# Kernel optimization log

Hardware: AMD Instinct MI355X
Metric: run time of the kernel (lower is better)

## Reference

```python
import jax, jax.numpy as jnp
import numpy as np

N = 100000   # nodes
E = 1600000  # edges (avg degree 16)
IN_DIM = 5
HID = 128
OUT_DIM = 1


def gcn_conv(x, src, dst, W, b, n):
    """PyG GCNConv: out = D^{-1/2}(A+I)D^{-1/2} (x @ W) + b, self-loops added."""
    h = x @ W  # [N, F_out]
    # degree including self-loop (edge weight 1 each)
    deg = jax.ops.segment_sum(jnp.ones(src.shape[0], h.dtype), dst, num_segments=n) + 1.0
    dinv = jax.lax.rsqrt(deg)  # deg >= 1 always (self-loop)
    coef = dinv[src] * dinv[dst]  # [E]
    agg = jax.ops.segment_sum(h[src] * coef[:, None], dst, num_segments=n)
    agg = agg + h * (dinv * dinv)[:, None]  # self-loop contribution
    return agg + b


def setup_inputs() -> dict:
    key = jax.random.key(0)
    k = jax.random.split(key, 6)
    x = jax.random.normal(k[0], (N, IN_DIM), jnp.float32)
    edge_index = jax.random.randint(k[1], (2, E), 0, N)
    W1 = jax.random.normal(k[2], (IN_DIM, HID), jnp.float32) / np.float32(np.sqrt(IN_DIM))
    b1 = jnp.zeros((HID,), jnp.float32)
    W2 = jax.random.normal(k[3], (HID, OUT_DIM), jnp.float32) / np.float32(np.sqrt(HID))
    b2 = jnp.zeros((OUT_DIM,), jnp.float32)
    return {"x": x, "edge_index": edge_index, "W1": W1, "b1": b1, "W2": W2, "b2": b2}


def reference(x, edge_index, W1, b1, W2, b2):
    src, dst = edge_index[0], edge_index[1]
    h = gcn_conv(x, src, dst, W1, b1, N)
    h = jax.nn.relu(h)
    out = gcn_conv(h, src, dst, W2, b2, N)
    return out
```

## Files before the change

### kernel.cpp

```cpp
#include <hip/hip_runtime.h>
#include <hip/hip_fp16.h>

#define Nn 100000
#define Ee 1600000
#define HID 128
#define IN_DIM 5

#define SH 8
#define BSZ 256
#define NB 391
#define BCAP 4608

#define PCHUNK 3125
#define PBLK 512
#define MAXK 7

typedef float f32x4 __attribute__((ext_vector_type(4)));
union F2H { float f; __half2 h; };

__global__ void zero_kernel(int* __restrict__ bcnt) {
    if (threadIdx.x < NB) bcnt[threadIdx.x] = 0;
}

__global__ __launch_bounds__(512) void partition_kernel(const int* __restrict__ src,
                                                        const int* __restrict__ dst,
                                                        unsigned int* __restrict__ recs,
                                                        int* __restrict__ bcnt) {
    __shared__ unsigned int stage[PCHUNK];
    __shared__ unsigned short bstage[PCHUNK];
    __shared__ int hist[NB + 1];
    __shared__ int histS[NB + 1];
    __shared__ int cur[NB];
    __shared__ int gbase[NB];
    __shared__ int wsum[8];
    int tid = threadIdx.x;
    int e0 = blockIdx.x * PCHUNK;
    for (int i = tid; i <= NB; i += 512) hist[i] = 0;
    __syncthreads();
    int rb[MAXK];
    unsigned int rv[MAXK];
    #pragma unroll
    for (int k = 0; k < MAXK; ++k) {
        int idx = tid + k * 512;
        rb[k] = -1;
        if (idx < PCHUNK) {
            int e = e0 + idx;
            int d = dst[e], s = src[e];
            rb[k] = d >> SH;
            rv[k] = ((unsigned int)(d & (BSZ - 1)) << 17) | (unsigned int)s;
            atomicAdd(&hist[rb[k]], 1);
        }
    }
    __syncthreads();
    int v = (tid < NB) ? hist[tid] : 0;
    int lane = tid & 63, wid = tid >> 6;
    int sc = v;
    #pragma unroll
    for (int ofs = 1; ofs < 64; ofs <<= 1) {
        int t = __shfl_up(sc, ofs, 64);
        if (lane >= ofs) sc += t;
    }
    if (lane == 63) wsum[wid] = sc;
    __syncthreads();
    int wpre = 0;
    #pragma unroll
    for (int w = 0; w < 8; ++w)
        if (w < wid) wpre += wsum[w];
    int excl = wpre + sc - v;
    if (tid < NB) {
        histS[tid] = excl;
        cur[tid] = excl;
        gbase[tid] = atomicAdd(&bcnt[tid], v);
    }
    __syncthreads();
    #pragma unroll
    for (int k = 0; k < MAXK; ++k)
        if (rb[k] >= 0) {
            int slot = atomicAdd(&cur[rb[k]], 1);
            stage[slot] = rv[k];
            bstage[slot] = (unsigned short)rb[k];
        }
    __syncthreads();
    for (int i = tid; i < PCHUNK; i += 512) {
        int b = bstage[i];
        recs[(size_t)b * BCAP + gbase[b] + (i - histS[b])] = stage[i];
    }
}

__global__ __launch_bounds__(BSZ) void sortk_kernel(const unsigned int* __restrict__ recs,
                                                    const int* __restrict__ bcnt,
                                                    const float* __restrict__ x,
                                                    int* __restrict__ degc,
                                                    unsigned int* __restrict__ nodeoff,
                                                    unsigned int* __restrict__ ssrc,
                                                    float* __restrict__ dinv,
                                                    f32x4* __restrict__ xd16) {
    __shared__ int cnt[BSZ];
    __shared__ int cur[BSZ];
    __shared__ int wsum[BSZ / 64];
    int b = blockIdx.x, tid = threadIdx.x;
    int n = bcnt[b];
    cnt[tid] = 0;
    __syncthreads();
    const unsigned int* R = recs + (size_t)b * BCAP;
    for (int i = tid; i < n; i += BSZ)
        atomicAdd(&cnt[R[i] >> 17], 1);
    __syncthreads();
    int v = cnt[tid];
    int lane = tid & 63, wid = tid >> 6;
    int sc = v;
    #pragma unroll
    for (int ofs = 1; ofs < 64; ofs <<= 1) {
        int t = __shfl_up(sc, ofs, 64);
        if (lane >= ofs) sc += t;
    }
    if (lane == 63) wsum[wid] = sc;
    __syncthreads();
    int wpre = 0;
    #pragma unroll
    for (int w = 0; w < BSZ / 64; ++w)
        if (w < wid) wpre += wsum[w];
    int excl = wpre + sc - v;
    cur[tid] = excl;
    int g = (b << SH) + tid;
    if (g < Nn) {
        degc[g] = v;
        nodeoff[g] = (unsigned int)(b * BCAP + excl);
        float di = rsqrtf((float)v + 1.0f);
        dinv[g] = di;
        f32x4 o;
        o.x = x[g * IN_DIM + 0] * di;
        o.y = x[g * IN_DIM + 1] * di;
        o.z = x[g * IN_DIM + 2] * di;
        F2H u;
        u.h = __floats2half2_rn(x[g * IN_DIM + 3] * di, x[g * IN_DIM + 4] * di);
        o.w = u.f;
        xd16[g] = o;
    }
    __syncthreads();
    unsigned int* O = ssrc + (size_t)b * BCAP;
    for (int i = tid; i < n; i += BSZ) {
        unsigned int r = R[i];
        int pos = atomicAdd(&cur[r >> 17], 1);
        O[pos] = r & 0x1FFFFu;
    }
}

__global__ __launch_bounds__(256) void gcn1_kernel(const unsigned int* __restrict__ ssrc,
                                                   const unsigned int* __restrict__ nodeoff,
                                                   const int* __restrict__ degc,
                                                   const f32x4* __restrict__ xd16,
                                                   const float* __restrict__ dinv,
                                                   const float* __restrict__ W1,
                                                   const float* __restrict__ b1,
                                                   const float* __restrict__ W2,
                                                   float* __restrict__ h2d) {
    __shared__ float w1s[IN_DIM * HID];
    __shared__ float w2s[HID], b1s[HID];
    int tid = threadIdx.x;
    for (int j = tid; j < IN_DIM * HID; j += 256) w1s[j] = W1[j];
    if (tid < HID) { w2s[tid] = W2[tid]; b1s[tid] = b1[tid]; }
    __syncthreads();
    int nd = blockIdx.x * 256 + tid;
    if (nd >= Nn) return;
    unsigned int off = nodeoff[nd];
    int len = degc[nd];
    float a0 = 0.f, a1 = 0.f, a2 = 0.f, a3 = 0.f, a4 = 0.f;
    int i = 0;
    for (; i + 4 <= len; i += 4) {
        unsigned int s0 = ssrc[off + i], s1 = ssrc[off + i + 1];
        unsigned int s2 = ssrc[off + i + 2], s3 = ssrc[off + i + 3];
        f32x4 v0 = xd16[s0], v1 = xd16[s1], v2 = xd16[s2], v3 = xd16[s3];
        F2H u0, u1, u2, u3;
        u0.f = v0.w; u1.f = v1.w; u2.f = v2.w; u3.f = v3.w;
        float2 e0 = __half22float2(u0.h), e1 = __half22float2(u1.h);
        float2 e2 = __half22float2(u2.h), e3 = __half22float2(u3.h);
        a0 += (v0.x + v1.x) + (v2.x + v3.x);
        a1 += (v0.y + v1.y) + (v2.y + v3.y);
        a2 += (v0.z + v1.z) + (v2.z + v3.z);
        a3 += (e0.x + e1.x) + (e2.x + e3.x);
        a4 += (e0.y + e1.y) + (e2.y + e3.y);
    }
    for (; i < len; ++i) {
        unsigned int s = ssrc[off + i];
        f32x4 v = xd16[s];
        F2H u; u.f = v.w; float2 e = __half22float2(u.h);
        a0 += v.x; a1 += v.y; a2 += v.z; a3 += e.x; a4 += e.y;
    }
    float di = dinv[nd];
    f32x4 sv = xd16[nd];
    F2H su; su.f = sv.w; float2 se = __half22float2(su.h);
    a0 = (a0 + sv.x) * di;
    a1 = (a1 + sv.y) * di;
    a2 = (a2 + sv.z) * di;
    a3 = (a3 + se.x) * di;
    a4 = (a4 + se.y) * di;
    float accp = 0.f;
    #pragma unroll
    for (int f = 0; f < HID; ++f) {
        float v = b1s[f] + a0 * w1s[f] + a1 * w1s[HID + f] + a2 * w1s[2 * HID + f]
                + a3 * w1s[3 * HID + f] + a4 * w1s[4 * HID + f];
        accp += fmaxf(v, 0.f) * w2s[f];
    }
    h2d[nd] = accp * di;
}

__global__ __launch_bounds__(256) void gcn2_kernel(const unsigned int* __restrict__ ssrc,
                                                   const unsigned int* __restrict__ nodeoff,
                                                   const int* __restrict__ degc,
                                                   const float* __restrict__ h2d,
                                                   const float* __restrict__ dinv,
                                                   const float* __restrict__ b2,
                                                   float* __restrict__ out) {
    int nd = blockIdx.x * 256 + threadIdx.x;
    if (nd >= Nn) return;
    unsigned int off = nodeoff[nd];
    int len = degc[nd];
    float s = 0.f;
    int i = 0;
    for (; i + 8 <= len; i += 8) {
        float t0 = h2d[ssrc[off + i]],     t1 = h2d[ssrc[off + i + 1]];
        float t2 = h2d[ssrc[off + i + 2]], t3 = h2d[ssrc[off + i + 3]];
        float t4 = h2d[ssrc[off + i + 4]], t5 = h2d[ssrc[off + i + 5]];
        float t6 = h2d[ssrc[off + i + 6]], t7 = h2d[ssrc[off + i + 7]];
        s += ((t0 + t1) + (t2 + t3)) + ((t4 + t5) + (t6 + t7));
    }
    for (; i < len; ++i) s += h2d[ssrc[off + i]];
    out[nd] = (s + h2d[nd]) * dinv[nd] + b2[0];
}

extern "C" void kernel_launch(void* const* d_in, const int* in_sizes, int n_in,
                              void* d_out, int out_size, void* d_ws, size_t ws_size,
                              hipStream_t stream) {
    const float* x  = (const float*)d_in[0];
    const int*   ei = (const int*)d_in[1];
    const float* W1 = (const float*)d_in[2];
    const float* b1 = (const float*)d_in[3];
    const float* W2 = (const float*)d_in[4];
    const float* b2 = (const float*)d_in[5];
    const int* src = ei;
    const int* dst = ei + Ee;
    float* out = (float*)d_out;

    float* dinv = (float*)d_ws;
    f32x4* xd16 = (f32x4*)(dinv + Nn);
    float* h2d  = (float*)(xd16 + Nn);
    int* degc   = (int*)(h2d + Nn);
    unsigned int* nodeoff = (unsigned int*)(degc + Nn);
    unsigned int* recs = nodeoff + Nn;
    unsigned int* ssrc = recs + (size_t)NB * BCAP;
    int* bcnt = (int*)(ssrc + (size_t)NB * BCAP);

    zero_kernel<<<1, 512, 0, stream>>>(bcnt);
    partition_kernel<<<PBLK, 512, 0, stream>>>(src, dst, recs, bcnt);
    sortk_kernel<<<NB, BSZ, 0, stream>>>(recs, bcnt, x, degc, nodeoff, ssrc, dinv, xd16);
    gcn1_kernel<<<(Nn + 255) / 256, 256, 0, stream>>>(ssrc, nodeoff, degc, xd16, dinv,
                                                      W1, b1, W2, h2d);
    gcn2_kernel<<<(Nn + 255) / 256, 256, 0, stream>>>(ssrc, nodeoff, degc, h2d, dinv, b2, out);
}
```

Measured before the change: 70.21 us.

## Build compact CSR via global degree atomics, block scan, and LDS-staged scatter

Per-node in-degrees are now counted with global atomics during partitioning instead of a per-bucket histogram pass. A new scan kernel assigns each 256-node block a base offset through an atomic allocator, giving a dense edge array with no per-bucket padding, and also computes dinv and the scaled features. The scatter kernel sorts bucket records into an LDS buffer and then writes them to global memory contiguously. The aim is to remove one read pass over the records, get coalesced writes and a compact CSR for the aggregation kernels. In exchange it adds 1.6M random global atomics and one more kernel launch.

```diff
diff --git a/kernel.cpp b/kernel.cpp
--- a/kernel.cpp
+++ b/kernel.cpp
@@ -18,12 +18,18 @@
 typedef float f32x4 __attribute__((ext_vector_type(4)));
 union F2H { float f; __half2 h; };
 
-__global__ void zero_kernel(int* __restrict__ bcnt) {
-    if (threadIdx.x < NB) bcnt[threadIdx.x] = 0;
+__global__ __launch_bounds__(256) void zero_kernel(int* __restrict__ degc,
+                                                   int* __restrict__ bcnt,
+                                                   unsigned int* __restrict__ galloc) {
+    int i = blockIdx.x * 256 + threadIdx.x;
+    if (i < Nn) degc[i] = 0;
+    if (i < NB) bcnt[i] = 0;
+    if (i == 0) *galloc = 0u;
 }
 
 __global__ __launch_bounds__(512) void partition_kernel(const int* __restrict__ src,
                                                         const int* __restrict__ dst,
+                                                        int* __restrict__ degc,
                                                         unsigned int* __restrict__ recs,
                                                         int* __restrict__ bcnt) {
     __shared__ unsigned int stage[PCHUNK];
@@ -46,6 +52,7 @@
         if (idx < PCHUNK) {
             int e = e0 + idx;
             int d = dst[e], s = src[e];
+            atomicAdd(&degc[d], 1);
             rb[k] = d >> SH;
             rv[k] = ((unsigned int)(d & (BSZ - 1)) << 17) | (unsigned int)s;
             atomicAdd(&hist[rb[k]], 1);
@@ -87,26 +94,17 @@
     }
 }
 
-__global__ __launch_bounds__(BSZ) void sortk_kernel(const unsigned int* __restrict__ recs,
-                                                    const int* __restrict__ bcnt,
-                                                    const float* __restrict__ x,
-                                                    int* __restrict__ degc,
-                                                    unsigned int* __restrict__ nodeoff,
-                                                    unsigned int* __restrict__ ssrc,
-                                                    float* __restrict__ dinv,
-                                                    f32x4* __restrict__ xd16) {
-    __shared__ int cnt[BSZ];
-    __shared__ int cur[BSZ];
-    __shared__ int wsum[BSZ / 64];
-    int b = blockIdx.x, tid = threadIdx.x;
-    int n = bcnt[b];
-    cnt[tid] = 0;
-    __syncthreads();
-    const unsigned int* R = recs + (size_t)b * BCAP;
-    for (int i = tid; i < n; i += BSZ)
-        atomicAdd(&cnt[R[i] >> 17], 1);
-    __syncthreads();
-    int v = cnt[tid];
+__global__ __launch_bounds__(256) void scan_prep_kernel(const int* __restrict__ degc,
+                                                        const float* __restrict__ x,
+                                                        unsigned int* __restrict__ nodeoff,
+                                                        float* __restrict__ dinv,
+                                                        f32x4* __restrict__ xd16,
+                                                        unsigned int* __restrict__ galloc) {
+    __shared__ int wsum[4];
+    __shared__ unsigned int bbase;
+    int tid = threadIdx.x;
+    int nd = blockIdx.x * 256 + tid;
+    int v = (nd < Nn) ? degc[nd] : 0;
     int lane = tid & 63, wid = tid >> 6;
     int sc = v;
     #pragma unroll
@@ -116,34 +114,63 @@
     }
     if (lane == 63) wsum[wid] = sc;
     __syncthreads();
+    if (tid == 0) {
+        int bt = wsum[0] + wsum[1] + wsum[2] + wsum[3];
+        bbase = atomicAdd(galloc, (unsigned int)bt);
+    }
+    __syncthreads();
     int wpre = 0;
     #pragma unroll
-    for (int w = 0; w < BSZ / 64; ++w)
+    for (int w = 0; w < 4; ++w)
         if (w < wid) wpre += wsum[w];
-    int excl = wpre + sc - v;
-    cur[tid] = excl;
+    if (nd < Nn) {
+        nodeoff[nd] = bbase + (unsigned int)(wpre + sc - v);
+        float di = rsqrtf((float)v + 1.0f);
+        dinv[nd] = di;
+        f32x4 o;
+        o.x = x[nd * IN_DIM + 0] * di;
+        o.y = x[nd * IN_DIM + 1] * di;
+        o.z = x[nd * IN_DIM + 2] * di;
+        F2H u;
+        u.h = __floats2half2_rn(x[nd * IN_DIM + 3] * di, x[nd * IN_DIM + 4] * di);
+        o.w = u.f;
+        xd16[nd] = o;
+    }
+}
+
+__global__ __launch_bounds__(BSZ) void scatter_kernel(const unsigned int* __restrict__ recs,
+                                                      const int* __restrict__ bcnt,
+                                                      const unsigned int* __restrict__ nodeoff,
+                                                      unsigned int* __restrict__ ssrc) {
+    __shared__ int cur[BSZ];
+    __shared__ unsigned int lstage[BCAP];
+    int b = blockIdx.x, tid = threadIdx.x;
+    int n = bcnt[b];
+    unsigned int bstart = nodeoff[(unsigned)(b << SH)];
     int g = (b << SH) + tid;
-    if (g < Nn) {
-        degc[g] = v;
-        nodeoff[g] = (unsigned int)(b * BCAP + excl);
-        float di = rsqrtf((float)v + 1.0f);
-        dinv[g] = di;
-        f32x4 o;
-        o.x = x[g * IN_DIM + 0] * di;
-        o.y = x[g * IN_DIM + 1] * di;
-        o.z = x[g * IN_DIM + 2] * di;
-        F2H u;
-        u.h = __floats2half2_rn(x[g * IN_DIM + 3] * di, x[g * IN_DIM + 4] * di);
-        o.w = u.f;
-        xd16[g] = o;
-    }
-    __syncthreads();
-    unsigned int* O = ssrc + (size_t)b * BCAP;
-    for (int i = tid; i < n; i += BSZ) {
+    cur[tid] = (g < Nn) ? (int)(nodeoff[g] - bstart) : 0;
+    __syncthreads();
+    const unsigned int* R = recs + (size_t)b * BCAP;
+    int i = tid;
+    for (; i + 3 * BSZ < n; i += 4 * BSZ) {
+        unsigned int r0 = R[i], r1 = R[i + BSZ], r2 = R[i + 2 * BSZ], r3 = R[i + 3 * BSZ];
+        int s0 = atomicAdd(&cur[r0 >> 17], 1);
+        int s1 = atomicAdd(&cur[r1 >> 17], 1);
+        int s2 = atomicAdd(&cur[r2 >> 17], 1);
+        int s3 = atomicAdd(&cur[r3 >> 17], 1);
+        lstage[s0] = r0 & 0x1FFFFu;
+        lstage[s1] = r1 & 0x1FFFFu;
+        lstage[s2] = r2 & 0x1FFFFu;
+        lstage[s3] = r3 & 0x1FFFFu;
+    }
+    for (; i < n; i += BSZ) {
         unsigned int r = R[i];
-        int pos = atomicAdd(&cur[r >> 17], 1);
-        O[pos] = r & 0x1FFFFu;
-    }
+        int slot = atomicAdd(&cur[r >> 17], 1);
+        lstage[slot] = r & 0x1FFFFu;
+    }
+    __syncthreads();
+    unsigned int* O = ssrc + bstart;
+    for (int j = tid; j < n; j += BSZ) O[j] = lstage[j];
 }
 
 __global__ __launch_bounds__(256) void gcn1_kernel(const unsigned int* __restrict__ ssrc,
@@ -249,11 +276,13 @@
     unsigned int* nodeoff = (unsigned int*)(degc + Nn);
     unsigned int* recs = nodeoff + Nn;
     unsigned int* ssrc = recs + (size_t)NB * BCAP;
-    int* bcnt = (int*)(ssrc + (size_t)NB * BCAP);
-
-    zero_kernel<<<1, 512, 0, stream>>>(bcnt);
-    partition_kernel<<<PBLK, 512, 0, stream>>>(src, dst, recs, bcnt);
-    sortk_kernel<<<NB, BSZ, 0, stream>>>(recs, bcnt, x, degc, nodeoff, ssrc, dinv, xd16);
+    int* bcnt = (int*)(ssrc + Ee);
+    unsigned int* galloc = (unsigned int*)(bcnt + NB);
+
+    zero_kernel<<<(Nn + 255) / 256, 256, 0, stream>>>(degc, bcnt, galloc);
+    partition_kernel<<<PBLK, 512, 0, stream>>>(src, dst, degc, recs, bcnt);
+    scan_prep_kernel<<<(Nn + 255) / 256, 256, 0, stream>>>(degc, x, nodeoff, dinv, xd16, galloc);
+    scatter_kernel<<<NB, BSZ, 0, stream>>>(recs, bcnt, nodeoff, ssrc);
     gcn1_kernel<<<(Nn + 255) / 256, 256, 0, stream>>>(ssrc, nodeoff, degc, xd16, dinv,
                                                       W1, b1, W2, h2d);
     gcn2_kernel<<<(Nn + 255) / 256, 256, 0, stream>>>(ssrc, nodeoff, degc, h2d, dinv, b2, out);
```

Result: slower. 129.1 us (+83.9%).
